# Kernel tuning notes

Hardware: AMD Instinct MI355X
Metric: run time of the kernel (lower is better)

## Reference

```python
import jax, jax.numpy as jnp
import numpy as np

OFFSETS = jnp.array([[-1, -1], [0, -1], [1, -1], [-1, 0], [0, 0], [1, 0],
                     [-1, 1], [0, 1], [1, 1]], dtype=jnp.float32)  # [9,2]
PIX_STEP = 2.0 / 96.0


def _bilinear_sample(img, gx, gy):
    """Bilinear grid_sample, padding_mode='zeros', align_corners=False.
    img: [B,H,W]; gx, gy: [B,P] in normalized coords [-1,1]. Returns [B,P]."""
    B, H, W = img.shape
    ix = ((gx + 1.0) * W - 1.0) * 0.5  # x indexes width
    iy = ((gy + 1.0) * H - 1.0) * 0.5
    x0f = jnp.floor(ix)
    y0f = jnp.floor(iy)
    wx = ix - x0f
    wy = iy - y0f
    x0 = x0f.astype(jnp.int32)
    y0 = y0f.astype(jnp.int32)
    x1 = x0 + 1
    y1 = y0 + 1
    flat = img.reshape(B, H * W)

    def gather(xi, yi):
        valid = (xi >= 0) & (xi < W) & (yi >= 0) & (yi < H)
        xc = jnp.clip(xi, 0, W - 1)
        yc = jnp.clip(yi, 0, H - 1)
        vals = jnp.take_along_axis(flat, yc * W + xc, axis=1)
        return jnp.where(valid, vals, 0.0)

    v00 = gather(x0, y0)
    v10 = gather(x1, y0)
    v01 = gather(x0, y1)
    v11 = gather(x1, y1)
    return (v00 * (1 - wx) * (1 - wy) + v10 * wx * (1 - wy)
            + v01 * (1 - wx) * wy + v11 * wx * wy)


def setup_inputs() -> dict:
    key = jax.random.key(0)
    k1, k2, k3 = jax.random.split(key, 3)
    B, N, H, W = 256, 16384, 96, 96
    corners = jax.random.uniform(k1, (B, N, 2), dtype=jnp.float32)
    edge_map = jax.random.uniform(k2, (B, 1, H, W), dtype=jnp.float32)
    mask_map = jax.random.uniform(k3, (B, 1, H, W), dtype=jnp.float32)
    return {"corners": corners, "edge_map": edge_map, "mask_map": mask_map}


def reference(corners, edge_map, mask_map):
    B, N, _ = corners.shape
    grid = corners * 2.0 - 1.0  # [B,N,2] (x,y)
    # 9-point neighborhood around each corner: [B,N,9,2]
    neigh = grid[:, :, None, :] + OFFSETS[None, None] * PIX_STEP
    gx = neigh[..., 0].reshape(B, N * 9)
    gy = neigh[..., 1].reshape(B, N * 9)
    sampled_edges = _bilinear_sample(edge_map[:, 0], gx, gy).reshape(B, N, 9)
    best_edge = jnp.max(sampled_edges, axis=-1)  # [B,N]
    edge_align_loss = jnp.mean(1.0 - best_edge)
    sampled_mask = _bilinear_sample(mask_map[:, 0], grid[..., 0], grid[..., 1])  # [B,N]
    mask_align_loss = jnp.mean((sampled_mask - 0.5) ** 2)
    return edge_align_loss + 2.0 * mask_align_loss
```

## Files before the change

kernel.cpp:

```cpp
#include <hip/hip_runtime.h>
#include <hip/hip_fp16.h>

constexpr int Bn = 256;
constexpr int Nn = 16384;
constexpr int Hh = 96;
constexpr int Ww = 96;

constexpr int THREADS = 1024;
constexpr int CHUNKS  = 2;
constexpr int EPS = 100;
constexpr int ESZ = 100 * 100;
constexpr int MPS = 50;
constexpr int MSZ = 100 * 50;
constexpr int PER_THREAD = Nn / CHUNKS / THREADS;

__global__ __launch_bounds__(THREADS, 8)
void geo_kernel(const float* __restrict__ corners,
                const float* __restrict__ edge,
                const float* __restrict__ mask,
                float2* __restrict__ partial)
{
    __shared__ alignas(16) __half2 sE[ESZ];
    __shared__ alignas(16) __half2 sM[MSZ];
    __shared__ float redE[THREADS / 64];
    __shared__ float redM[THREADS / 64];

    const int b     = blockIdx.x >> 1;
    const int chunk = blockIdx.x & 1;
    const int tid   = threadIdx.x;

    const float4* c4 =
        (const float4*)(corners + (size_t)b * Nn * 2 + (size_t)chunk * (Nn / CHUNKS) * 2);
    float4 cc[4];
#pragma unroll
    for (int k = 0; k < 4; ++k)
        cc[k] = c4[k * THREADS + tid];

    {
        const __half2 z2 = __float22half2_rn(make_float2(0.f, 0.f));
        if (tid < 400) sE[(tid < 200) ? tid : (9600 + tid)] = z2;
        if (tid < 288) {
            int r = tid / 3;
            int k = tid - 3 * r;
            int c = (k == 0) ? 0 : (97 + k);
            sE[(r + 2) * EPS + c] = z2;
        }
        if (tid < 200) sM[(tid < 100) ? tid : (4800 + tid)] = z2;
        if (tid < 192) {
            int r = tid >> 1;
            int c = (tid & 1) ? 49 : 0;
            sM[(r + 2) * MPS + c] = z2;
        }
    }

    {
        const float* ebase = edge + (size_t)b * Hh * Ww;
        const float* mbase = mask + (size_t)b * Hh * Ww;
        for (int i = tid; i < Hh * (Ww / 2); i += THREADS) {
            int r = i / (Ww / 2);
            int j = i - r * (Ww / 2);
            const float* erow = ebase + r * Ww;
            float2 ae = *(const float2*)(erow + 2 * j);
            float ne = (2 * j + 2 < Ww) ? erow[2 * j + 2] : 0.f;
            int base = (r + 2) * EPS + 2 * j + 2;
            sE[base]     = __float22half2_rn(make_float2(ae.x, ae.y));
            sE[base + 1] = __float22half2_rn(make_float2(ae.y, ne));
            if (j == 0)
                sE[(r + 2) * EPS + 1] = __float22half2_rn(make_float2(0.f, ae.x));
            float2 am = *(const float2*)(mbase + r * Ww + 2 * j);
            sM[(r + 2) * MPS + 1 + j] = __float22half2_rn(make_float2(am.x, am.y));
        }
    }
    __syncthreads();

    float eAcc = 0.f, mAcc = 0.f;
#pragma unroll
    for (int jj = 0; jj < PER_THREAD; ++jj) {
        float cx = (jj & 1) ? ((jj & 2) ? cc[jj >> 1].z : cc[jj >> 1].z)
                            : cc[jj >> 1].x;
        float cy;
        if (jj & 1) { cx = cc[jj >> 1].z; cy = cc[jj >> 1].w; }
        else        { cx = cc[jj >> 1].x; cy = cc[jj >> 1].y; }
        float ix = fmaf(cx, 96.f, -0.5f);
        float iy = fmaf(cy, 96.f, -0.5f);
        float x0f = floorf(ix), y0f = floorf(iy);
        float wx = ix - x0f, wy = iy - y0f;
        int x0 = (int)x0f, y0 = (int)y0f;

        int cb = (y0 + 1) * EPS + (x0 + 1);
        __half2 e00 = sE[cb],           e01 = sE[cb + 2];
        __half2 e10 = sE[cb + EPS],     e11 = sE[cb + EPS + 2];
        __half2 e20 = sE[cb + 2 * EPS], e21 = sE[cb + 2 * EPS + 2];
        __half2 e30 = sE[cb + 3 * EPS], e31 = sE[cb + 3 * EPS + 2];

        int e0  = (x0 + 2) >> 1;
        int odd = x0 & 1;
        int mb  = (y0 + 2) * MPS + e0;
        __half2 ma_lo = sM[mb],       ma_hi = sM[mb + 1];
        __half2 mc_lo = sM[mb + MPS], mc_hi = sM[mb + MPS + 1];

        float2 r00 = __half22float2(e00), r01 = __half22float2(e01);
        float2 r10 = __half22float2(e10), r11 = __half22float2(e11);
        float2 r20 = __half22float2(e20), r21 = __half22float2(e21);
        float2 r30 = __half22float2(e30), r31 = __half22float2(e31);

        float h[4][3];
        h[0][0] = fmaf(wx, r00.y - r00.x, r00.x);
        h[0][1] = fmaf(wx, r01.x - r00.y, r00.y);
        h[0][2] = fmaf(wx, r01.y - r01.x, r01.x);
        h[1][0] = fmaf(wx, r10.y - r10.x, r10.x);
        h[1][1] = fmaf(wx, r11.x - r10.y, r10.y);
        h[1][2] = fmaf(wx, r11.y - r11.x, r11.x);
        h[2][0] = fmaf(wx, r20.y - r20.x, r20.x);
        h[2][1] = fmaf(wx, r21.x - r20.y, r20.y);
        h[2][2] = fmaf(wx, r21.y - r21.x, r21.x);
        h[3][0] = fmaf(wx, r30.y - r30.x, r30.x);
        h[3][1] = fmaf(wx, r31.x - r30.y, r30.y);
        h[3][2] = fmaf(wx, r31.y - r31.x, r31.x);

        float best = fmaf(wy, h[1][0] - h[0][0], h[0][0]);
#pragma unroll
        for (int r = 0; r < 3; ++r) {
#pragma unroll
            for (int k = 0; k < 3; ++k) {
                if (r == 0 && k == 0) continue;
                float s = fmaf(wy, h[r + 1][k] - h[r][k], h[r][k]);
                best = fmaxf(best, s);
            }
        }
        eAcc += best;

        float2 qa = __half22float2(ma_lo), qb = __half22float2(ma_hi);
        float2 qc = __half22float2(mc_lo), qd = __half22float2(mc_hi);
        float l0 = odd ? qa.y : qa.x;
        float r0 = odd ? qb.x : qa.y;
        float l1 = odd ? qc.y : qc.x;
        float r1 = odd ? qd.x : qc.y;
        float t = fmaf(wx, r0 - l0, l0);
        float u = fmaf(wx, r1 - l1, l1);
        float m = fmaf(wy, u - t, t);
        float d = m - 0.5f;
        mAcc = fmaf(d, d, mAcc);
    }

#pragma unroll
    for (int off = 32; off > 0; off >>= 1) {
        eAcc += __shfl_xor(eAcc, off);
        mAcc += __shfl_xor(mAcc, off);
    }
    const int wv = tid >> 6;
    const int ln = tid & 63;
    if (ln == 0) { redE[wv] = eAcc; redM[wv] = mAcc; }
    __syncthreads();

    if (tid == 0) {
        float e = 0.f, m = 0.f;
#pragma unroll
        for (int w = 0; w < THREADS / 64; ++w) { e += redE[w]; m += redM[w]; }
        partial[blockIdx.x] = make_float2(e, m);
    }
}

__global__ __launch_bounds__(512)
void geo_reduce(const float2* __restrict__ partial, float* __restrict__ out)
{
    __shared__ double rE[8];
    __shared__ double rM[8];
    const int tid = threadIdx.x;
    float2 p = partial[tid];
    double e = (double)p.x, m = (double)p.y;
#pragma unroll
    for (int off = 32; off > 0; off >>= 1) {
        e += __shfl_xor(e, off);
        m += __shfl_xor(m, off);
    }
    if ((tid & 63) == 0) { rE[tid >> 6] = e; rM[tid >> 6] = m; }
    __syncthreads();
    if (tid == 0) {
        double se = 0.0, sm = 0.0;
#pragma unroll
        for (int w = 0; w < 8; ++w) { se += rE[w]; sm += rM[w]; }
        const double inv = 1.0 / (double)((long long)Bn * (long long)Nn);
        double edge_loss = 1.0 - se * inv;
        double mask_loss = sm * inv;
        out[0] = (float)(edge_loss + 2.0 * mask_loss);
    }
}

extern "C" void kernel_launch(void* const* d_in, const int* in_sizes, int n_in,
                              void* d_out, int out_size, void* d_ws, size_t ws_size,
                              hipStream_t stream)
{
    const float* corners = (const float*)d_in[0];
    const float* edge    = (const float*)d_in[1];
    const float* mask    = (const float*)d_in[2];
    float* out      = (float*)d_out;
    float2* partial = (float2*)d_ws;

    geo_kernel<<<Bn * CHUNKS, THREADS, 0, stream>>>(corners, edge, mask, partial);
    geo_reduce<<<1, 512, 0, stream>>>(partial, out);
}
```

Measured before the change: 28.97 us.

## Use packed fp16 edge interpolation, overlapping mask layout, and four chunks per image

```diff
diff --git a/kernel.cpp b/kernel.cpp
--- a/kernel.cpp
+++ b/kernel.cpp
@@ -6,27 +6,34 @@
 constexpr int Hh = 96;
 constexpr int Ww = 96;
 
-constexpr int THREADS = 1024;
-constexpr int CHUNKS  = 2;
-constexpr int EPS = 100;
-constexpr int ESZ = 100 * 100;
-constexpr int MPS = 50;
-constexpr int MSZ = 100 * 50;
+constexpr int THREADS = 512;
+constexpr int CHUNKS  = 4;
 constexpr int PER_THREAD = Nn / CHUNKS / THREADS;
 
-__global__ __launch_bounds__(THREADS, 8)
+constexpr int MOFF = 10000;
+constexpr int TOTENT = 10000 + 9800;
+
+static __device__ inline __half2 pkmax2(__half2 a, __half2 b)
+{
+    unsigned int ai = *(unsigned int*)&a;
+    unsigned int bi = *(unsigned int*)&b;
+    unsigned int ri;
+    asm("v_pk_max_f16 %0, %1, %2" : "=v"(ri) : "v"(ai), "v"(bi));
+    return *(__half2*)&ri;
+}
+
+__global__ __launch_bounds__(THREADS, 4)
 void geo_kernel(const float* __restrict__ corners,
                 const float* __restrict__ edge,
                 const float* __restrict__ mask,
                 float2* __restrict__ partial)
 {
-    __shared__ alignas(16) __half2 sE[ESZ];
-    __shared__ alignas(16) __half2 sM[MSZ];
+    __shared__ __half2 sB[TOTENT];
     __shared__ float redE[THREADS / 64];
     __shared__ float redM[THREADS / 64];
 
-    const int b     = blockIdx.x >> 1;
-    const int chunk = blockIdx.x & 1;
+    const int b     = blockIdx.x >> 2;
+    const int chunk = blockIdx.x & 3;
     const int tid   = threadIdx.x;
 
     const float4* c4 =
@@ -37,19 +44,20 @@
         cc[k] = c4[k * THREADS + tid];
 
     {
-        const __half2 z2 = __float22half2_rn(make_float2(0.f, 0.f));
-        if (tid < 400) sE[(tid < 200) ? tid : (9600 + tid)] = z2;
-        if (tid < 288) {
-            int r = tid / 3;
-            int k = tid - 3 * r;
-            int c = (k == 0) ? 0 : (97 + k);
-            sE[(r + 2) * EPS + c] = z2;
-        }
-        if (tid < 200) sM[(tid < 100) ? tid : (4800 + tid)] = z2;
-        if (tid < 192) {
-            int r = tid >> 1;
-            int c = (tid & 1) ? 49 : 0;
-            sM[(r + 2) * MPS + c] = z2;
+        const __half2 z2 = __halves2half2(__ushort_as_half(0), __ushort_as_half(0));
+        for (int i = tid; i < 1176; i += THREADS) {
+            int idx;
+            if (i < 200)        idx = i;
+            else if (i < 400)   idx = 9600 + i;
+            else if (i < 500)   idx = MOFF + (i - 400);
+            else if (i < 600)   idx = MOFF + 9200 + i;
+            else if (i < 888) { int k = i - 600; int r = k / 3; int c = k - 3 * r;
+                                c = (c == 0) ? 0 : (97 + c);
+                                idx = (r + 2) * 100 + c; }
+            else              { int k = i - 888; int r = k / 3; int c = k - 3 * r;
+                                c = (c == 0) ? 0 : (97 + c);
+                                idx = MOFF + (r + 1) * 100 + c; }
+            sB[idx] = z2;
         }
     }
 
@@ -60,15 +68,21 @@
             int r = i / (Ww / 2);
             int j = i - r * (Ww / 2);
             const float* erow = ebase + r * Ww;
+            const float* mrow = mbase + r * Ww;
             float2 ae = *(const float2*)(erow + 2 * j);
+            float2 am = *(const float2*)(mrow + 2 * j);
             float ne = (2 * j + 2 < Ww) ? erow[2 * j + 2] : 0.f;
-            int base = (r + 2) * EPS + 2 * j + 2;
-            sE[base]     = __float22half2_rn(make_float2(ae.x, ae.y));
-            sE[base + 1] = __float22half2_rn(make_float2(ae.y, ne));
-            if (j == 0)
-                sE[(r + 2) * EPS + 1] = __float22half2_rn(make_float2(0.f, ae.x));
-            float2 am = *(const float2*)(mbase + r * Ww + 2 * j);
-            sM[(r + 2) * MPS + 1 + j] = __float22half2_rn(make_float2(am.x, am.y));
+            float nm = (2 * j + 2 < Ww) ? mrow[2 * j + 2] : 0.f;
+            int eb2 = (r + 2) * 100 + 2 * j + 2;
+            sB[eb2]     = __float22half2_rn(make_float2(ae.x, ae.y));
+            sB[eb2 + 1] = __float22half2_rn(make_float2(ae.y, ne));
+            int mb2 = MOFF + (r + 1) * 100 + 2 * j + 2;
+            sB[mb2]     = __float22half2_rn(make_float2(am.x, am.y));
+            sB[mb2 + 1] = __float22half2_rn(make_float2(am.y, nm));
+            if (j == 0) {
+                sB[(r + 2) * 100 + 1]        = __float22half2_rn(make_float2(0.f, ae.x));
+                sB[MOFF + (r + 1) * 100 + 1] = __float22half2_rn(make_float2(0.f, am.x));
+            }
         }
     }
     __syncthreads();
@@ -76,71 +90,68 @@
     float eAcc = 0.f, mAcc = 0.f;
 #pragma unroll
     for (int jj = 0; jj < PER_THREAD; ++jj) {
-        float cx = (jj & 1) ? ((jj & 2) ? cc[jj >> 1].z : cc[jj >> 1].z)
-                            : cc[jj >> 1].x;
-        float cy;
-        if (jj & 1) { cx = cc[jj >> 1].z; cy = cc[jj >> 1].w; }
-        else        { cx = cc[jj >> 1].x; cy = cc[jj >> 1].y; }
+        float4 q = cc[jj >> 1];
+        float cx = (jj & 1) ? q.z : q.x;
+        float cy = (jj & 1) ? q.w : q.y;
         float ix = fmaf(cx, 96.f, -0.5f);
         float iy = fmaf(cy, 96.f, -0.5f);
         float x0f = floorf(ix), y0f = floorf(iy);
         float wx = ix - x0f, wy = iy - y0f;
         int x0 = (int)x0f, y0 = (int)y0f;
 
-        int cb = (y0 + 1) * EPS + (x0 + 1);
-        __half2 e00 = sE[cb],           e01 = sE[cb + 2];
-        __half2 e10 = sE[cb + EPS],     e11 = sE[cb + EPS + 2];
-        __half2 e20 = sE[cb + 2 * EPS], e21 = sE[cb + 2 * EPS + 2];
-        __half2 e30 = sE[cb + 3 * EPS], e31 = sE[cb + 3 * EPS + 2];
-
-        int e0  = (x0 + 2) >> 1;
-        int odd = x0 & 1;
-        int mb  = (y0 + 2) * MPS + e0;
-        __half2 ma_lo = sM[mb],       ma_hi = sM[mb + 1];
-        __half2 mc_lo = sM[mb + MPS], mc_hi = sM[mb + MPS + 1];
-
-        float2 r00 = __half22float2(e00), r01 = __half22float2(e01);
-        float2 r10 = __half22float2(e10), r11 = __half22float2(e11);
-        float2 r20 = __half22float2(e20), r21 = __half22float2(e21);
-        float2 r30 = __half22float2(e30), r31 = __half22float2(e31);
-
-        float h[4][3];
-        h[0][0] = fmaf(wx, r00.y - r00.x, r00.x);
-        h[0][1] = fmaf(wx, r01.x - r00.y, r00.y);
-        h[0][2] = fmaf(wx, r01.y - r01.x, r01.x);
-        h[1][0] = fmaf(wx, r10.y - r10.x, r10.x);
-        h[1][1] = fmaf(wx, r11.x - r10.y, r10.y);
-        h[1][2] = fmaf(wx, r11.y - r11.x, r11.x);
-        h[2][0] = fmaf(wx, r20.y - r20.x, r20.x);
-        h[2][1] = fmaf(wx, r21.x - r20.y, r20.y);
-        h[2][2] = fmaf(wx, r21.y - r21.x, r21.x);
-        h[3][0] = fmaf(wx, r30.y - r30.x, r30.x);
-        h[3][1] = fmaf(wx, r31.x - r30.y, r30.y);
-        h[3][2] = fmaf(wx, r31.y - r31.x, r31.x);
-
-        float best = fmaf(wy, h[1][0] - h[0][0], h[0][0]);
-#pragma unroll
-        for (int r = 0; r < 3; ++r) {
-#pragma unroll
-            for (int k = 0; k < 3; ++k) {
-                if (r == 0 && k == 0) continue;
-                float s = fmaf(wy, h[r + 1][k] - h[r][k], h[r][k]);
-                best = fmaxf(best, s);
-            }
+        int v   = y0 * 100 + x0;
+        int cb  = v + 101;
+        int cb3 = v + 401;
+        int mb  = v + MOFF + 102;
+
+        __half2 e00 = sB[cb],        e01 = sB[cb + 2];
+        __half2 e10 = sB[cb + 100],  e11 = sB[cb + 102];
+        __half2 e20 = sB[cb + 200],  e21 = sB[cb + 202];
+        __half2 e30 = sB[cb3],       e31 = sB[cb3 + 2];
+        __half2 ma  = sB[mb],        mc  = sB[mb + 100];
+
+        const __half2 wx2 = __half2half2(__float2half_rn(wx));
+        const __half2 wy2 = __half2half2(__float2half_rn(wy));
+
+        __half2 hL0, hL1, hL2, hL3, hR0, hR1, hR2, hR3;
+        {
+            __half2 s, d;
+            s = __halves2half2(__high2half(e00), __low2half(e01));
+            hL0 = __hfma2(wx2, __hsub2(s, e00), e00);
+            d = __half2half2(__high2half(e01));
+            hR0 = __hfma2(wx2, __hsub2(d, e01), e01);
+            s = __halves2half2(__high2half(e10), __low2half(e11));
+            hL1 = __hfma2(wx2, __hsub2(s, e10), e10);
+            d = __half2half2(__high2half(e11));
+            hR1 = __hfma2(wx2, __hsub2(d, e11), e11);
+            s = __halves2half2(__high2half(e20), __low2half(e21));
+            hL2 = __hfma2(wx2, __hsub2(s, e20), e20);
+            d = __half2half2(__high2half(e21));
+            hR2 = __hfma2(wx2, __hsub2(d, e21), e21);
+            s = __halves2half2(__high2half(e30), __low2half(e31));
+            hL3 = __hfma2(wx2, __hsub2(s, e30), e30);
+            d = __half2half2(__high2half(e31));
+            hR3 = __hfma2(wx2, __hsub2(d, e31), e31);
         }
-        eAcc += best;
-
-        float2 qa = __half22float2(ma_lo), qb = __half22float2(ma_hi);
-        float2 qc = __half22float2(mc_lo), qd = __half22float2(mc_hi);
-        float l0 = odd ? qa.y : qa.x;
-        float r0 = odd ? qb.x : qa.y;
-        float l1 = odd ? qc.y : qc.x;
-        float r1 = odd ? qd.x : qc.y;
-        float t = fmaf(wx, r0 - l0, l0);
-        float u = fmaf(wx, r1 - l1, l1);
+        __half2 vL0 = __hfma2(wy2, __hsub2(hL1, hL0), hL0);
+        __half2 vL1 = __hfma2(wy2, __hsub2(hL2, hL1), hL1);
+        __half2 vL2 = __hfma2(wy2, __hsub2(hL3, hL2), hL2);
+        __half2 vR0 = __hfma2(wy2, __hsub2(hR1, hR0), hR0);
+        __half2 vR1 = __hfma2(wy2, __hsub2(hR2, hR1), hR1);
+        __half2 vR2 = __hfma2(wy2, __hsub2(hR3, hR2), hR2);
+        __half2 mL = pkmax2(pkmax2(vL0, vL1), vL2);
+        __half2 mR = pkmax2(pkmax2(vR0, vR1), vR2);
+        __half best_h = __hmax(__hmax(__low2half(mL), __high2half(mL)),
+                               __low2half(mR));
+        eAcc += __half2float(best_h);
+
+        float2 qa = __half22float2(ma);
+        float2 qc = __half22float2(mc);
+        float t = fmaf(wx, qa.y - qa.x, qa.x);
+        float u = fmaf(wx, qc.y - qc.x, qc.x);
         float m = fmaf(wy, u - t, t);
-        float d = m - 0.5f;
-        mAcc = fmaf(d, d, mAcc);
+        float dd = m - 0.5f;
+        mAcc = fmaf(dd, dd, mAcc);
     }
 
 #pragma unroll
@@ -161,11 +172,11 @@
     }
 }
 
-__global__ __launch_bounds__(512)
+__global__ __launch_bounds__(1024)
 void geo_reduce(const float2* __restrict__ partial, float* __restrict__ out)
 {
-    __shared__ double rE[8];
-    __shared__ double rM[8];
+    __shared__ double rE[16];
+    __shared__ double rM[16];
     const int tid = threadIdx.x;
     float2 p = partial[tid];
     double e = (double)p.x, m = (double)p.y;
@@ -179,7 +190,7 @@
     if (tid == 0) {
         double se = 0.0, sm = 0.0;
 #pragma unroll
-        for (int w = 0; w < 8; ++w) { se += rE[w]; sm += rM[w]; }
+        for (int w = 0; w < 16; ++w) { se += rE[w]; sm += rM[w]; }
         const double inv = 1.0 / (double)((long long)Bn * (long long)Nn);
         double edge_loss = 1.0 - se * inv;
         double mask_loss = sm * inv;
@@ -198,5 +209,5 @@
     float2* partial = (float2*)d_ws;
 
     geo_kernel<<<Bn * CHUNKS, THREADS, 0, stream>>>(corners, edge, mask, partial);
-    geo_reduce<<<1, 512, 0, stream>>>(partial, out);
-}
+    geo_reduce<<<1, 1024, 0, stream>>>(partial, out);
+}
```

Measured after the change: 39.23 us. 1.35x slower.
